# Kernel tuning notes

Hardware: AMD Instinct MI355X
Metric: run time of the kernel (lower is better)

## Reference

```python
import jax, jax.numpy as jnp
import numpy as np

B, N, D_IN, D_H, D_OUT = 32, 512, 512, 512, 512


def _xavier(key, fan_in, fan_out):
    bound = np.sqrt(6.0 / (fan_in + fan_out))
    return jax.random.uniform(key, (fan_in, fan_out), jnp.float32, -bound, bound)


def setup_inputs() -> dict:
    key = jax.random.key(0)
    ks = jax.random.split(key, 8)
    batch_graph = jax.random.normal(ks[0], (B, N, D_IN), jnp.float32)
    adj = jax.random.uniform(ks[1], (B, N, N), jnp.float32)  # per-graph adjacency blocks
    W0 = _xavier(ks[2], D_IN, D_H)
    b0 = jnp.zeros((D_H,), jnp.float32)
    W1 = _xavier(ks[3], D_H, D_H)
    b1 = jnp.zeros((D_H,), jnp.float32)
    W2 = _xavier(ks[4], D_H, D_OUT)
    b2 = jnp.zeros((D_OUT,), jnp.float32)
    return {"batch_graph": batch_graph, "adj": adj,
            "W0": W0, "b0": b0, "W1": W1, "b1": b1, "W2": W2, "b2": b2}


def _gcn_layer(h, adj, W, b):
    # GraphConvolution: adj @ (h @ W) + b, batched per graph.
    # Equivalent to big_adj @ (big_graph @ W) since big_adj is block-diagonal.
    support = jnp.einsum('bnd,de->bne', h, W)
    return jnp.einsum('bnm,bme->bne', adj, support) + b


def reference(batch_graph, adj, W0, b0, W1, b1, W2, b2):
    # dropout is identity at inference time
    h = jax.nn.relu(_gcn_layer(batch_graph, adj, W0, b0))
    h = jax.nn.relu(_gcn_layer(h, adj, W1, b1))
    h = _gcn_layer(h, adj, W2, b2)  # no activation on final layer
    return h  # [B, N, D_OUT] == torch.stack(big_graph.split(N))
```

## Files before the change

### kernel.cpp

```cpp
#include <hip/hip_runtime.h>
#include <stdint.h>

typedef __bf16 bf16x8 __attribute__((ext_vector_type(8)));
typedef float f32x4 __attribute__((ext_vector_type(4)));
typedef unsigned short u16x4 __attribute__((ext_vector_type(4)));

static __device__ __forceinline__ unsigned short f2bf(float f) {
    union { float f; unsigned u; } v; v.f = f;
    unsigned r = (v.u + 0x7FFFu + ((v.u >> 16) & 1u)) >> 16;
    return (unsigned short)r;
}

__global__ void prep_kernel(const float* __restrict__ X,
                            const float* __restrict__ adj,
                            const float* __restrict__ W0,
                            const float* __restrict__ W1,
                            const float* __restrict__ W2,
                            unsigned short* __restrict__ bufH,
                            unsigned short* __restrict__ adjB,
                            unsigned short* __restrict__ Wt) {
    const int bid = blockIdx.x;
    const int t = threadIdx.x;
    if (bid < 16384) {
        const float* src = (bid < 8192) ? X : adj;
        unsigned short* dst = (bid < 8192) ? bufH : adjB;
        const int i = (bid & 8191) * 256 + t;
        f32x4 v = ((const f32x4*)src)[i];
        u16x4 o;
        o.x = f2bf(v.x); o.y = f2bf(v.y); o.z = f2bf(v.z); o.w = f2bf(v.w);
        ((u16x4*)dst)[i] = o;
    } else {
        const int wb = bid - 16384;
        const int z = wb >> 8;
        const int tile = wb & 255;
        const float* W = (z == 0) ? W0 : (z == 1) ? W1 : W2;
        unsigned short* out = Wt + (size_t)z * (512 * 512);
        __shared__ float tileS[32][33];
        const int bx = (tile & 15) * 32, by = (tile >> 4) * 32;
        const int tx = t & 31, ty = t >> 5;
        #pragma unroll
        for (int r = 0; r < 32; r += 8)
            tileS[ty + r][tx] = W[(size_t)(by + ty + r) * 512 + (bx + tx)];
        __syncthreads();
        #pragma unroll
        for (int r = 0; r < 32; r += 8)
            out[(size_t)(bx + ty + r) * 512 + (by + tx)] = f2bf(tileS[tx][ty + r]);
    }
}

template<int LDA, int LDB, int LDO, bool BIAS, bool RELU, typename OT>
__global__ __launch_bounds__(256, 2)
void gemm_abT_ct(const unsigned short* __restrict__ A,
                 const unsigned short* __restrict__ B,
                 OT* __restrict__ out, const float* __restrict__ bias,
                 long batchA, long batchB, long batchO) {
    __shared__ unsigned short As[128 * 128];
    __shared__ unsigned short Bs[128 * 128];

    const int tid  = threadIdx.x;
    const int lane = tid & 63;
    const int wave = tid >> 6;
    const int quad = lane >> 4;
    const int l16  = lane & 15;
    const int wm   = wave & 1;
    const int wn   = wave >> 1;

    const int m0 = blockIdx.x * 128;
    const int n0 = blockIdx.y * 128;
    A   += (size_t)blockIdx.z * batchA;
    B   += (size_t)blockIdx.z * batchB;
    out += (size_t)blockIdx.z * batchO;

    const int trow = tid >> 4;
    const int tpos = (tid & 15) ^ trow;
    const unsigned short* aG = A + (size_t)(m0 + trow) * LDA + tpos * 8;
    const unsigned short* bG = B + (size_t)(n0 + trow) * LDB + tpos * 8;
    char* aL = (char*)As + tid * 16;
    char* bL = (char*)Bs + tid * 16;

    f32x4 acc[4][4];
    #pragma unroll
    for (int i = 0; i < 4; ++i)
        #pragma unroll
        for (int j = 0; j < 4; ++j) {
            f32x4 z = {0.f, 0.f, 0.f, 0.f};
            acc[i][j] = z;
        }

    #pragma unroll 1
    for (int kk = 0; kk < 4; ++kk) {
        const int ko = kk * 128;
        #pragma unroll
        for (int r = 0; r < 8; ++r) {
            __builtin_amdgcn_global_load_lds(
                (__attribute__((address_space(1))) void*)(uintptr_t)(aG + (size_t)(r * 16) * LDA + ko),
                (__attribute__((address_space(3))) void*)(aL + r * 4096), 16, 0, 0);
        }
        #pragma unroll
        for (int r = 0; r < 8; ++r) {
            __builtin_amdgcn_global_load_lds(
                (__attribute__((address_space(1))) void*)(uintptr_t)(bG + (size_t)(r * 16) * LDB + ko),
                (__attribute__((address_space(3))) void*)(bL + r * 4096), 16, 0, 0);
        }
        __syncthreads();

        #pragma unroll
        for (int ks = 0; ks < 4; ++ks) {
            bf16x8 af[4], bfr[4];
            #pragma unroll
            for (int i = 0; i < 4; ++i) {
                const int row = wm * 64 + i * 16 + l16;
                const int idx = row * 16 + ((ks * 4 + quad) ^ (row & 15));
                af[i] = *(const bf16x8*)((const char*)As + idx * 16);
            }
            #pragma unroll
            for (int j = 0; j < 4; ++j) {
                const int row = wn * 64 + j * 16 + l16;
                const int idx = row * 16 + ((ks * 4 + quad) ^ (row & 15));
                bfr[j] = *(const bf16x8*)((const char*)Bs + idx * 16);
            }
            #pragma unroll
            for (int i = 0; i < 4; ++i)
                #pragma unroll
                for (int j = 0; j < 4; ++j)
                    acc[i][j] = __builtin_amdgcn_mfma_f32_16x16x32_bf16(af[i], bfr[j], acc[i][j], 0, 0, 0);
        }
        __syncthreads();
    }

    #pragma unroll
    for (int i = 0; i < 4; ++i) {
        const int mb = m0 + wm * 64 + i * 16 + quad * 4;
        f32x4 bb = {0.f, 0.f, 0.f, 0.f};
        if constexpr (BIAS) bb = *(const f32x4*)(bias + mb);
        #pragma unroll
        for (int j = 0; j < 4; ++j) {
            const int n = n0 + wn * 64 + j * 16 + l16;
            f32x4 v = acc[i][j];
            if constexpr (BIAS) v += bb;
            if constexpr (RELU) {
                v.x = v.x > 0.f ? v.x : 0.f;
                v.y = v.y > 0.f ? v.y : 0.f;
                v.z = v.z > 0.f ? v.z : 0.f;
                v.w = v.w > 0.f ? v.w : 0.f;
            }
            if constexpr (sizeof(OT) == 4) {
                *(f32x4*)((float*)out + (size_t)n * LDO + mb) = v;
            } else {
                u16x4 o;
                o.x = f2bf(v.x); o.y = f2bf(v.y); o.z = f2bf(v.z); o.w = f2bf(v.w);
                *(u16x4*)((unsigned short*)out + (size_t)n * LDO + mb) = o;
            }
        }
    }
}

extern "C" void kernel_launch(void* const* d_in, const int* in_sizes, int n_in,
                              void* d_out, int out_size, void* d_ws, size_t ws_size,
                              hipStream_t stream) {
    (void)in_sizes; (void)n_in; (void)out_size; (void)ws_size;
    const float* X   = (const float*)d_in[0];
    const float* adj = (const float*)d_in[1];
    const float* W0  = (const float*)d_in[2];
    const float* b0  = (const float*)d_in[3];
    const float* W1  = (const float*)d_in[4];
    const float* b1  = (const float*)d_in[5];
    const float* W2  = (const float*)d_in[6];
    const float* b2  = (const float*)d_in[7];
    float* out = (float*)d_out;

    char* ws = (char*)d_ws;
    const size_t SZ = 16777216;
    unsigned short* adjB = (unsigned short*)(ws);
    unsigned short* bufH = (unsigned short*)(ws + SZ);
    unsigned short* tmpT = (unsigned short*)(ws + 2 * SZ);
    unsigned short* Wt   = (unsigned short*)(ws + 3 * SZ);
    const unsigned short* W0t = Wt;
    const unsigned short* W1t = Wt + 262144;
    const unsigned short* W2t = Wt + 2 * 262144;

    prep_kernel<<<16384 + 768, 256, 0, stream>>>(X, adj, W0, W1, W2, bufH, adjB, Wt);

    const long BATCH = 512L * 512L;

    gemm_abT_ct<512, 512, 16384, false, false, unsigned short>
        <<<dim3(128, 4, 1), 256, 0, stream>>>(bufH, W0t, tmpT, nullptr, 0, 0, 0);
    gemm_abT_ct<16384, 512, 512, true, true, unsigned short>
        <<<dim3(4, 4, 32), 256, 0, stream>>>(tmpT, adjB, bufH, b0, 512, BATCH, BATCH);
    gemm_abT_ct<512, 512, 16384, false, false, unsigned short>
        <<<dim3(128, 4, 1), 256, 0, stream>>>(bufH, W1t, tmpT, nullptr, 0, 0, 0);
    gemm_abT_ct<16384, 512, 512, true, true, unsigned short>
        <<<dim3(4, 4, 32), 256, 0, stream>>>(tmpT, adjB, bufH, b1, 512, BATCH, BATCH);
    gemm_abT_ct<512, 512, 16384, false, false, unsigned short>
        <<<dim3(128, 4, 1), 256, 0, stream>>>(bufH, W2t, tmpT, nullptr, 0, 0, 0);
    gemm_abT_ct<16384, 512, 512, true, false, float>
        <<<dim3(4, 4, 32), 256, 0, stream>>>(tmpT, adjB, out, b2, 512, BATCH, BATCH);
}
```

Baseline: 223.0 us.

## Fuse both GEMMs of each GCN layer into one kernel via LDS

Each GCN layer now runs as a single kernel. A block loads a 64-column slice of the transposed weights into LDS, computes the support slice for one graph, writes it back to LDS as bf16, then multiplies by that graph's adjacency, with bias and ReLU applied in the epilogue. This removes the global round trip of the support tensor and halves the number of launches. The cost is that the h and adj operands are read straight from global memory without LDS staging or double-buffering. The grid is also only 256 blocks of 512 threads at one block per CU, which may limit latency hiding.

```diff
diff --git a/kernel.cpp b/kernel.cpp
--- a/kernel.cpp
+++ b/kernel.cpp
@@ -1,5 +1,8 @@
 #include <hip/hip_runtime.h>
 #include <stdint.h>
+
+#define AS1 __attribute__((address_space(1)))
+#define AS3 __attribute__((address_space(3)))
 
 typedef __bf16 bf16x8 __attribute__((ext_vector_type(8)));
 typedef float f32x4 __attribute__((ext_vector_type(4)));
@@ -34,7 +37,7 @@
         const int z = wb >> 8;
         const int tile = wb & 255;
         const float* W = (z == 0) ? W0 : (z == 1) ? W1 : W2;
-        unsigned short* out = Wt + (size_t)z * (512 * 512);
+        unsigned short* dst = Wt + (size_t)z * (512 * 512);
         __shared__ float tileS[32][33];
         const int bx = (tile & 15) * 32, by = (tile >> 4) * 32;
         const int tx = t & 31, ty = t >> 5;
@@ -44,39 +47,47 @@
         __syncthreads();
         #pragma unroll
         for (int r = 0; r < 32; r += 8)
-            out[(size_t)(bx + ty + r) * 512 + (by + tx)] = f2bf(tileS[tx][ty + r]);
-    }
-}
-
-template<int LDA, int LDB, int LDO, bool BIAS, bool RELU, typename OT>
-__global__ __launch_bounds__(256, 2)
-void gemm_abT_ct(const unsigned short* __restrict__ A,
-                 const unsigned short* __restrict__ B,
-                 OT* __restrict__ out, const float* __restrict__ bias,
-                 long batchA, long batchB, long batchO) {
-    __shared__ unsigned short As[128 * 128];
-    __shared__ unsigned short Bs[128 * 128];
+            dst[(size_t)(bx + ty + r) * 512 + (by + tx)] = f2bf(tileS[tx][ty + r]);
+    }
+}
+
+template<bool RELU, typename OT>
+__global__ __launch_bounds__(512, 1)
+void gcn_layer(const unsigned short* __restrict__ hin,
+               const unsigned short* __restrict__ adjB,
+               const unsigned short* __restrict__ WtL,
+               const float* __restrict__ bias,
+               OT* __restrict__ hout) {
+    __shared__ unsigned short AM[32768];
+
+    const int bid = blockIdx.x;
+    const int s = bid >> 3;
+    const int g = (bid & 7) + 8 * (s >> 3);
+    const int e0 = (s & 7) * 64;
+
+    const unsigned short* __restrict__ h_g = hin + (size_t)g * 262144;
+    const unsigned short* __restrict__ a_g = adjB + (size_t)g * 262144;
 
     const int tid  = threadIdx.x;
     const int lane = tid & 63;
-    const int wave = tid >> 6;
+    const int w    = tid >> 6;
     const int quad = lane >> 4;
     const int l16  = lane & 15;
-    const int wm   = wave & 1;
-    const int wn   = wave >> 1;
-
-    const int m0 = blockIdx.x * 128;
-    const int n0 = blockIdx.y * 128;
-    A   += (size_t)blockIdx.z * batchA;
-    B   += (size_t)blockIdx.z * batchB;
-    out += (size_t)blockIdx.z * batchO;
-
-    const int trow = tid >> 4;
-    const int tpos = (tid & 15) ^ trow;
-    const unsigned short* aG = A + (size_t)(m0 + trow) * LDA + tpos * 8;
-    const unsigned short* bG = B + (size_t)(n0 + trow) * LDB + tpos * 8;
-    char* aL = (char*)As + tid * 16;
-    char* bL = (char*)Bs + tid * 16;
+    const int n0w  = w * 64;
+
+    {
+        const int row = (tid & 255) >> 2;
+        const int pos = (tid & 3) ^ ((tid >> 2) & 3);
+        const unsigned short* gsrc =
+            WtL + (size_t)(e0 + row) * 512 + (tid >> 8) * 32 + pos * 8;
+        char* ldst = (char*)AM + tid * 16;
+        #pragma unroll
+        for (int r = 0; r < 8; ++r)
+            __builtin_amdgcn_global_load_lds(
+                (AS1 void*)(uintptr_t)(gsrc + r * 64),
+                (AS3 void*)(ldst + r * 8192), 16, 0, 0);
+    }
+    __syncthreads();
 
     f32x4 acc[4][4];
     #pragma unroll
@@ -87,57 +98,82 @@
             acc[i][j] = z;
         }
 
-    #pragma unroll 1
-    for (int kk = 0; kk < 4; ++kk) {
-        const int ko = kk * 128;
-        #pragma unroll
-        for (int r = 0; r < 8; ++r) {
-            __builtin_amdgcn_global_load_lds(
-                (__attribute__((address_space(1))) void*)(uintptr_t)(aG + (size_t)(r * 16) * LDA + ko),
-                (__attribute__((address_space(3))) void*)(aL + r * 4096), 16, 0, 0);
-        }
-        #pragma unroll
-        for (int r = 0; r < 8; ++r) {
-            __builtin_amdgcn_global_load_lds(
-                (__attribute__((address_space(1))) void*)(uintptr_t)(bG + (size_t)(r * 16) * LDB + ko),
-                (__attribute__((address_space(3))) void*)(bL + r * 4096), 16, 0, 0);
-        }
-        __syncthreads();
-
-        #pragma unroll
-        for (int ks = 0; ks < 4; ++ks) {
-            bf16x8 af[4], bfr[4];
+    #pragma unroll
+    for (int kb = 0; kb < 16; ++kb) {
+        bf16x8 af[4], bf[4];
+        #pragma unroll
+        for (int i = 0; i < 4; ++i) {
+            const int row = i * 16 + l16;
+            af[i] = *(const bf16x8*)((char*)AM + kb * 4096 +
+                                     (row * 4 + (quad ^ (row & 3))) * 16);
+        }
+        #pragma unroll
+        for (int j = 0; j < 4; ++j)
+            bf[j] = *(const bf16x8*)(h_g + (size_t)(n0w + j * 16 + l16) * 512 +
+                                     kb * 32 + quad * 8);
+        #pragma unroll
+        for (int i = 0; i < 4; ++i)
             #pragma unroll
-            for (int i = 0; i < 4; ++i) {
-                const int row = wm * 64 + i * 16 + l16;
-                const int idx = row * 16 + ((ks * 4 + quad) ^ (row & 15));
-                af[i] = *(const bf16x8*)((const char*)As + idx * 16);
+            for (int j = 0; j < 4; ++j)
+                acc[i][j] = __builtin_amdgcn_mfma_f32_16x16x32_bf16(af[i], bf[j], acc[i][j], 0, 0, 0);
+    }
+    __syncthreads();
+
+    #pragma unroll
+    for (int i = 0; i < 4; ++i)
+        #pragma unroll
+        for (int j = 0; j < 4; ++j) {
+            const int m = n0w + j * 16 + l16;
+            const int mb = m >> 5;
+            const int q = (m >> 3) & 3;
+            const int elem = m & 7;
+            #pragma unroll
+            for (int r = 0; r < 4; ++r) {
+                const int e = i * 16 + quad * 4 + r;
+                *((unsigned short*)((char*)AM + mb * 4096 +
+                                    (e * 4 + (q ^ (e & 3))) * 16) + elem)
+                    = f2bf(acc[i][j][r]);
             }
+        }
+    __syncthreads();
+
+    f32x4 acc2[4][4];
+    #pragma unroll
+    for (int i = 0; i < 4; ++i)
+        #pragma unroll
+        for (int j = 0; j < 4; ++j) {
+            f32x4 z = {0.f, 0.f, 0.f, 0.f};
+            acc2[i][j] = z;
+        }
+
+    #pragma unroll
+    for (int mb = 0; mb < 16; ++mb) {
+        bf16x8 af[4], bf[4];
+        #pragma unroll
+        for (int i = 0; i < 4; ++i) {
+            const int row = i * 16 + l16;
+            af[i] = *(const bf16x8*)((char*)AM + mb * 4096 +
+                                     (row * 4 + (quad ^ (row & 3))) * 16);
+        }
+        #pragma unroll
+        for (int j = 0; j < 4; ++j)
+            bf[j] = *(const bf16x8*)(a_g + (size_t)(n0w + j * 16 + l16) * 512 +
+                                     mb * 32 + quad * 8);
+        #pragma unroll
+        for (int i = 0; i < 4; ++i)
             #pragma unroll
-            for (int j = 0; j < 4; ++j) {
-                const int row = wn * 64 + j * 16 + l16;
-                const int idx = row * 16 + ((ks * 4 + quad) ^ (row & 15));
-                bfr[j] = *(const bf16x8*)((const char*)Bs + idx * 16);
-            }
-            #pragma unroll
-            for (int i = 0; i < 4; ++i)
-                #pragma unroll
-                for (int j = 0; j < 4; ++j)
-                    acc[i][j] = __builtin_amdgcn_mfma_f32_16x16x32_bf16(af[i], bfr[j], acc[i][j], 0, 0, 0);
-        }
-        __syncthreads();
+            for (int j = 0; j < 4; ++j)
+                acc2[i][j] = __builtin_amdgcn_mfma_f32_16x16x32_bf16(af[i], bf[j], acc2[i][j], 0, 0, 0);
     }
 
     #pragma unroll
     for (int i = 0; i < 4; ++i) {
-        const int mb = m0 + wm * 64 + i * 16 + quad * 4;
-        f32x4 bb = {0.f, 0.f, 0.f, 0.f};
-        if constexpr (BIAS) bb = *(const f32x4*)(bias + mb);
-        #pragma unroll
-        for (int j = 0; j < 4; ++j) {
-            const int n = n0 + wn * 64 + j * 16 + l16;
-            f32x4 v = acc[i][j];
-            if constexpr (BIAS) v += bb;
+        const int e = e0 + i * 16 + quad * 4;
+        const f32x4 bb = *(const f32x4*)(bias + e);
+        #pragma unroll
+        for (int j = 0; j < 4; ++j) {
+            const int n = n0w + j * 16 + l16;
+            f32x4 v = acc2[i][j] + bb;
             if constexpr (RELU) {
                 v.x = v.x > 0.f ? v.x : 0.f;
                 v.y = v.y > 0.f ? v.y : 0.f;
@@ -145,11 +181,11 @@
                 v.w = v.w > 0.f ? v.w : 0.f;
             }
             if constexpr (sizeof(OT) == 4) {
-                *(f32x4*)((float*)out + (size_t)n * LDO + mb) = v;
+                *(f32x4*)((float*)hout + (size_t)g * 262144 + (size_t)n * 512 + e) = v;
             } else {
                 u16x4 o;
                 o.x = f2bf(v.x); o.y = f2bf(v.y); o.z = f2bf(v.z); o.w = f2bf(v.w);
-                *(u16x4*)((unsigned short*)out + (size_t)n * LDO + mb) = o;
+                *(u16x4*)((unsigned short*)hout + (size_t)g * 262144 + (size_t)n * 512 + e) = o;
             }
         }
     }
@@ -171,28 +207,17 @@
 
     char* ws = (char*)d_ws;
     const size_t SZ = 16777216;
-    unsigned short* adjB = (unsigned short*)(ws);
-    unsigned short* bufH = (unsigned short*)(ws + SZ);
-    unsigned short* tmpT = (unsigned short*)(ws + 2 * SZ);
-    unsigned short* Wt   = (unsigned short*)(ws + 3 * SZ);
-    const unsigned short* W0t = Wt;
-    const unsigned short* W1t = Wt + 262144;
-    const unsigned short* W2t = Wt + 2 * 262144;
+    unsigned short* adjB  = (unsigned short*)(ws);
+    unsigned short* bufH  = (unsigned short*)(ws + SZ);
+    unsigned short* bufH2 = (unsigned short*)(ws + 2 * SZ);
+    unsigned short* Wt    = (unsigned short*)(ws + 3 * SZ);
 
     prep_kernel<<<16384 + 768, 256, 0, stream>>>(X, adj, W0, W1, W2, bufH, adjB, Wt);
 
-    const long BATCH = 512L * 512L;
-
-    gemm_abT_ct<512, 512, 16384, false, false, unsigned short>
-        <<<dim3(128, 4, 1), 256, 0, stream>>>(bufH, W0t, tmpT, nullptr, 0, 0, 0);
-    gemm_abT_ct<16384, 512, 512, true, true, unsigned short>
-        <<<dim3(4, 4, 32), 256, 0, stream>>>(tmpT, adjB, bufH, b0, 512, BATCH, BATCH);
-    gemm_abT_ct<512, 512, 16384, false, false, unsigned short>
-        <<<dim3(128, 4, 1), 256, 0, stream>>>(bufH, W1t, tmpT, nullptr, 0, 0, 0);
-    gemm_abT_ct<16384, 512, 512, true, true, unsigned short>
-        <<<dim3(4, 4, 32), 256, 0, stream>>>(tmpT, adjB, bufH, b1, 512, BATCH, BATCH);
-    gemm_abT_ct<512, 512, 16384, false, false, unsigned short>
-        <<<dim3(128, 4, 1), 256, 0, stream>>>(bufH, W2t, tmpT, nullptr, 0, 0, 0);
-    gemm_abT_ct<16384, 512, 512, true, false, float>
-        <<<dim3(4, 4, 32), 256, 0, stream>>>(tmpT, adjB, out, b2, 512, BATCH, BATCH);
-}
+    gcn_layer<true, unsigned short>
+        <<<256, 512, 0, stream>>>(bufH, adjB, Wt, b0, bufH2);
+    gcn_layer<true, unsigned short>
+        <<<256, 512, 0, stream>>>(bufH2, adjB, Wt + 262144, b1, bufH);
+    gcn_layer<false, float>
+        <<<256, 512, 0, stream>>>(bufH, adjB, Wt + 2 * 262144, b2, out);
+}
```

After: 229.1 us. 2.7% more time.
